# Kernel tuning notes

Hardware: AMD Instinct MI355X
Metric: run time of the kernel (lower is better)

The kernel has to match this reference:

```python
import jax, jax.numpy as jnp
import numpy as np

D_MODEL, H, D_FF = 1024, 16, 4096
D_K = D_MODEL // H
EPS = 1e-6
NEG = -1e9


def _layer_norm(x, alpha, bias):
    # torch LayerNormalization: scalar alpha/bias, unbiased std (ddof=1), eps added to std
    n = x.shape[-1]
    mu = jnp.mean(x, axis=-1, keepdims=True)
    var = jnp.sum((x - mu) ** 2, axis=-1, keepdims=True) / (n - 1)
    std = jnp.sqrt(var)
    return alpha * (x - mu) / (std + EPS) + bias


def _linear(x, w, b):
    # torch nn.Linear: y = x @ W^T + b, W: [out, in]
    return jnp.einsum('bsd,od->bso', x, w) + b


def setup_inputs() -> dict:
    key = jax.random.key(0)
    ks = jax.random.split(key, 12)
    d, dff = D_MODEL, D_FF
    s_d = 1.0 / np.sqrt(d)
    s_ff = 1.0 / np.sqrt(dff)
    inp = {
        'x': jax.random.normal(ks[0], (2, 2048, d), dtype=jnp.float32),
        'mask': jnp.ones((2, 1, 1, 2048), dtype=jnp.int32),
        'wq': jax.random.uniform(ks[1], (d, d), jnp.float32, -s_d, s_d),
        'bq': jnp.zeros((d,), jnp.float32),
        'wk': jax.random.uniform(ks[2], (d, d), jnp.float32, -s_d, s_d),
        'bk': jnp.zeros((d,), jnp.float32),
        'wv': jax.random.uniform(ks[3], (d, d), jnp.float32, -s_d, s_d),
        'bv': jnp.zeros((d,), jnp.float32),
        'wo': jax.random.uniform(ks[4], (d, d), jnp.float32, -s_d, s_d),
        'bo': jnp.zeros((d,), jnp.float32),
        'w1': jax.random.uniform(ks[5], (dff, d), jnp.float32, -s_d, s_d),
        'b1': jnp.zeros((dff,), jnp.float32),
        'w2': jax.random.uniform(ks[6], (d, dff), jnp.float32, -s_ff, s_ff),
        'b2': jnp.zeros((d,), jnp.float32),
        'ln1_a': jnp.ones((1,), jnp.float32),
        'ln1_b': jnp.zeros((1,), jnp.float32),
        'ln2_a': jnp.ones((1,), jnp.float32),
        'ln2_b': jnp.zeros((1,), jnp.float32),
    }
    return inp


def reference(x, mask, wq, bq, wk, bk, wv, bv, wo, bo, w1, b1, w2, b2,
              ln1_a, ln1_b, ln2_a, ln2_b):
    b, s, d = x.shape

    # --- residual 1: pre-norm self-attention (dropout is identity in eval) ---
    xn = _layer_norm(x, ln1_a, ln1_b)
    q = _linear(xn, wq, bq).reshape(b, s, H, D_K).transpose(0, 2, 1, 3)  # [b,h,s,dk]
    k = _linear(xn, wk, bk).reshape(b, s, H, D_K).transpose(0, 2, 1, 3)
    v = _linear(xn, wv, bv).reshape(b, s, H, D_K).transpose(0, 2, 1, 3)
    scores = jnp.einsum('bhqd,bhkd->bhqk', q, k) / jnp.sqrt(jnp.float32(D_K))
    scores = jnp.where(mask == 0, NEG, scores)
    p = jax.nn.softmax(scores, axis=-1)
    attn = jnp.einsum('bhqk,bhkd->bhqd', p, v)
    attn = attn.transpose(0, 2, 1, 3).reshape(b, s, d)
    x = x + _linear(attn, wo, bo)

    # --- residual 2: pre-norm feed-forward ---
    xn = _layer_norm(x, ln2_a, ln2_b)
    h = jax.nn.relu(_linear(xn, w1, b1))
    x = x + _linear(h, w2, b2)
    return x
```

## Files before the change

kernel.cpp:

```cpp
#include <hip/hip_runtime.h>
#include <hip/hip_bf16.h>
#include <stdint.h>

typedef __bf16 bf16x8 __attribute__((ext_vector_type(8)));
typedef __bf16 bf16x4 __attribute__((ext_vector_type(4)));
typedef short  s16x4  __attribute__((ext_vector_type(4)));
typedef float  f32x4  __attribute__((ext_vector_type(4)));
typedef unsigned short u16;

__device__ __forceinline__ u16 f2bf(float f) {
    return __builtin_bit_cast(u16, (__bf16)f);
}

__device__ __forceinline__ f32x4 vmax4(f32x4 a, f32x4 b) {
    f32x4 r;
    r[0] = fmaxf(a[0], b[0]); r[1] = fmaxf(a[1], b[1]);
    r[2] = fmaxf(a[2], b[2]); r[3] = fmaxf(a[3], b[3]);
    return r;
}
__device__ __forceinline__ f32x4 vexp4(f32x4 a) {
    f32x4 r;
    r[0] = __expf(a[0]); r[1] = __expf(a[1]);
    r[2] = __expf(a[2]); r[3] = __expf(a[3]);
    return r;
}

__device__ __forceinline__ f32x4 mfma16(bf16x4 a, bf16x4 b, f32x4 c) {
#if __has_builtin(__builtin_amdgcn_mfma_f32_16x16x16bf16_1k)
    return __builtin_amdgcn_mfma_f32_16x16x16bf16_1k(
        __builtin_bit_cast(s16x4, a), __builtin_bit_cast(s16x4, b), c, 0, 0, 0);
#else
    f32x4 d;
    asm volatile("v_mfma_f32_16x16x16_bf16 %0, %1, %2, %3"
                 : "=v"(d) : "v"(a), "v"(b), "v"(c));
    return d;
#endif
}

__device__ __forceinline__ void stage16(const void* g, void* lds_wave_base) {
#if __has_builtin(__builtin_amdgcn_global_load_lds)
    __builtin_amdgcn_global_load_lds(
        (const __attribute__((address_space(1))) void*)g,
        (__attribute__((address_space(3))) void*)lds_wave_base, 16, 0, 0);
#else
    int lane = threadIdx.x & 63;
    *(uint4*)((char*)lds_wave_base + lane * 16) = *(const uint4*)g;
#endif
}

__device__ __forceinline__ int swz(int r) {
    return (((r) & 7) ^ (((r) >> 3) & 7)) << 4;
}

__global__ void pack1_kernel(const float* __restrict__ wq, const float* __restrict__ wk,
                             const float* __restrict__ wv, const float* __restrict__ bq,
                             const float* __restrict__ bk, const float* __restrict__ bv,
                             const float* __restrict__ wo,
                             u16* __restrict__ wqkv, float* __restrict__ bqkv,
                             u16* __restrict__ wo_b) {
    size_t i0 = (size_t)blockIdx.x * 256 + threadIdx.x;
    size_t stride = (size_t)gridDim.x * 256;
    const size_t DD = 1024u * 1024u;
    for (size_t i = i0; i < 3 * DD; i += stride) {
        float v;
        if (i < DD)          v = wq[i] * 0.125f;
        else if (i < 2 * DD) v = wk[i - DD];
        else                 v = wv[i - 2 * DD];
        wqkv[i] = f2bf(v);
    }
    for (size_t i = i0; i < DD; i += stride) wo_b[i] = f2bf(wo[i]);
    for (size_t i = i0; i < 3072; i += stride)
        bqkv[i] = (i < 1024) ? bq[i] * 0.125f : ((i < 2048) ? bk[i - 1024] : bv[i - 2048]);
}

__global__ void pack2_kernel(const float* __restrict__ w1, const float* __restrict__ w2,
                             u16* __restrict__ w1_b, u16* __restrict__ w2_b) {
    size_t i0 = (size_t)blockIdx.x * 256 + threadIdx.x;
    size_t stride = (size_t)gridDim.x * 256;
    const size_t DD = 1024u * 1024u;
    for (size_t i = i0; i < 4 * DD; i += stride) w1_b[i] = f2bf(w1[i]);
    for (size_t i = i0; i < 4 * DD; i += stride) w2_b[i] = f2bf(w2[i]);
}

__global__ __launch_bounds__(256)
void ln_kernel(const float* __restrict__ x, u16* __restrict__ out,
               const float* __restrict__ alpha, const float* __restrict__ beta) {
    const int row = blockIdx.x;
    const int t = threadIdx.x, lane = t & 63, w = t >> 6;
    float4 v = ((const float4*)(x + (size_t)row * 1024))[t];
    float s  = v.x + v.y + v.z + v.w;
    float ss = v.x * v.x + v.y * v.y + v.z * v.z + v.w * v.w;
#pragma unroll
    for (int d = 1; d < 64; d <<= 1) { s += __shfl_xor(s, d); ss += __shfl_xor(ss, d); }
    __shared__ float red[8];
    if (lane == 0) { red[w] = s; red[4 + w] = ss; }
    __syncthreads();
    s  = red[0] + red[1] + red[2] + red[3];
    ss = red[4] + red[5] + red[6] + red[7];
    const float mu  = s * (1.f / 1024.f);
    const float var = fmaxf((ss - 1024.f * mu * mu) * (1.f / 1023.f), 0.f);
    const float inv = alpha[0] / (sqrtf(var) + 1e-6f);
    const float bb  = beta[0];
    ushort4 o;
    o.x = f2bf((v.x - mu) * inv + bb);
    o.y = f2bf((v.y - mu) * inv + bb);
    o.z = f2bf((v.z - mu) * inv + bb);
    o.w = f2bf((v.w - mu) * inv + bb);
    ((ushort4*)(out + (size_t)row * 1024))[t] = o;
}

template <int EPI>
__global__ __launch_bounds__(256)
void gemm_bt(const u16* __restrict__ A, const u16* __restrict__ B,
             const float* __restrict__ bias, const float* __restrict__ resid,
             void* __restrict__ Cout, int M, int N, int K, int ldc) {
    __shared__ __align__(16) char As[8192];
    __shared__ __align__(16) char Bs[8192];
    const int t = threadIdx.x;
    const int lane = t & 63, wave = t >> 6;
    const int g = lane >> 4, c = lane & 15;
    const int wm = wave >> 1, wn = wave & 1;
    const int bm = blockIdx.x, bn = blockIdx.y;

    const f32x4 z4 = {0.f, 0.f, 0.f, 0.f};
    f32x4 acc[4][4];
#pragma unroll
    for (int m = 0; m < 4; ++m)
#pragma unroll
        for (int n = 0; n < 4; ++n) acc[m][n] = z4;

    const int srow = t >> 2;
    const int ak = (((t & 3) ^ ((t >> 2) & 3)) << 3);
    const u16* ga = A + (size_t)(bm * 128 + srow) * K + ak;
    const u16* gb = B + (size_t)(bn * 128 + srow) * K + ak;
    char* la = As + wave * 1024;
    char* lb = Bs + wave * 1024;
    const size_t rstep = (size_t)64 * K;

    for (int k0 = 0; k0 < K; k0 += 32) {
        __syncthreads();
        stage16(ga + k0,         la);
        stage16(ga + k0 + rstep, la + 4096);
        stage16(gb + k0,         lb);
        stage16(gb + k0 + rstep, lb + 4096);
        __syncthreads();
        bf16x8 a[4], b[4];
#pragma unroll
        for (int m = 0; m < 4; ++m) {
            int r = wm * 64 + m * 16 + c;
            a[m] = *(const bf16x8*)(As + r * 64 + ((g * 16) ^ ((c & 3) << 4)));
        }
#pragma unroll
        for (int n = 0; n < 4; ++n) {
            int r = wn * 64 + n * 16 + c;
            b[n] = *(const bf16x8*)(Bs + r * 64 + ((g * 16) ^ ((c & 3) << 4)));
        }
#pragma unroll
        for (int m = 0; m < 4; ++m)
#pragma unroll
            for (int n = 0; n < 4; ++n)
                acc[m][n] = __builtin_amdgcn_mfma_f32_16x16x32_bf16(a[m], b[n], acc[m][n], 0, 0, 0);
    }

    const int row0 = bm * 128 + wm * 64;
    const int col0 = bn * 128 + wn * 64;
#pragma unroll
    for (int m = 0; m < 4; ++m) {
#pragma unroll
        for (int n = 0; n < 4; ++n) {
            const int cc = col0 + n * 16 + c;
            const float bv = bias[cc];
#pragma unroll
            for (int j = 0; j < 4; ++j) {
                const int rr = row0 + m * 16 + g * 4 + j;
                float v = acc[m][n][j] + bv;
                if (EPI == 1) v = v > 0.f ? v : 0.f;
                if (EPI == 2) {
                    ((float*)Cout)[(size_t)rr * ldc + cc] = resid[(size_t)rr * ldc + cc] + v;
                } else {
                    ((u16*)Cout)[(size_t)rr * ldc + cc] = f2bf(v);
                }
            }
        }
    }
}

__global__ __launch_bounds__(256)
void attn_kernel(const u16* __restrict__ qkv, const int* __restrict__ mask,
                 u16* __restrict__ attn_out) {
    __shared__ __align__(16) char Ksm[32768];
    __shared__ __align__(16) char Vsm[32768];
    const int t = threadIdx.x, lane = t & 63, w = t >> 6;
    const int g = lane >> 4, c = lane & 15;
    const int flat = blockIdx.x;
    const int xcd = flat & 7, u = flat >> 3;
    const int qt = u & 15;
    const int p = xcd * 4 + (u >> 4);
    const int h = p & 15, b = p >> 4;
    const int S = 2048, LD = 3072;
    const int NT = S / 128;

    bf16x8 qf[2][2];
#pragma unroll
    for (int m = 0; m < 2; ++m)
#pragma unroll
        for (int half = 0; half < 2; ++half)
            qf[m][half] = *(const bf16x8*)&qkv[(size_t)(b * S + qt * 128 + w * 32 + m * 16 + c) * LD
                                               + h * 64 + half * 32 + g * 8];

    const f32x4 z4 = {0.f, 0.f, 0.f, 0.f};
    f32x4 accO[2][4];
#pragma unroll
    for (int m = 0; m < 2; ++m)
#pragma unroll
        for (int dt = 0; dt < 4; ++dt) accO[m][dt] = z4;
    float mrun[2] = {-1e30f, -1e30f};
    float lrun[2] = {0.f, 0.f};

    unsigned vr[2][8];
    const int vd0 = (t & 31) * 2;
    const int vkg[2] = {t >> 5, 8 + (t >> 5)};

    auto STAGEK = [&](int kt, char* Kd) {
#pragma unroll
        for (int it = 0; it < 4; ++it) {
            int idx = it * 256 + t;
            int k = idx >> 3, pp = idx & 7;
            int ps = pp ^ ((k & 7) ^ ((k >> 3) & 7));
            stage16(&qkv[(size_t)(b * S + kt * 128 + k) * LD + 1024 + h * 64 + ps * 8],
                    Kd + (it * 256 + w * 64) * 16);
        }
    };
    auto VLOAD = [&](int kt) {
#pragma unroll
        for (int it = 0; it < 2; ++it) {
            const u16* src = &qkv[(size_t)(b * S + kt * 128 + vkg[it] * 8) * LD + 2048 + h * 64 + vd0];
#pragma unroll
            for (int i = 0; i < 8; ++i)
                vr[it][i] = *(const unsigned*)(src + (size_t)i * LD);
        }
    };
    auto VWRITE = [&](char* Vd) {
#pragma unroll
        for (int it = 0; it < 2; ++it) {
            int d0 = vd0, kg = vkg[it];
            uint4 lo, hi;
            lo.x = (vr[it][0] & 0xffffu) | (vr[it][1] << 16);
            lo.y = (vr[it][2] & 0xffffu) | (vr[it][3] << 16);
            lo.z = (vr[it][4] & 0xffffu) | (vr[it][5] << 16);
            lo.w = (vr[it][6] & 0xffffu) | (vr[it][7] << 16);
            hi.x = (vr[it][0] >> 16) | (vr[it][1] & 0xffff0000u);
            hi.y = (vr[it][2] >> 16) | (vr[it][3] & 0xffff0000u);
            hi.z = (vr[it][4] >> 16) | (vr[it][5] & 0xffff0000u);
            hi.w = (vr[it][6] >> 16) | (vr[it][7] & 0xffff0000u);
            *(uint4*)(Vd + d0 * 256 + ((kg * 16) ^ swz(d0)))           = lo;
            *(uint4*)(Vd + (d0 + 1) * 256 + ((kg * 16) ^ swz(d0 + 1))) = hi;
        }
    };

    STAGEK(0, Ksm);
    VLOAD(0);
    asm volatile("s_waitcnt vmcnt(0)" ::: "memory");
    VWRITE(Vsm);
    __syncthreads();

    int cur = 0;
    for (int kt = 0; kt < NT; ++kt) {
        char* Kc = Ksm + cur * 16384;
        char* Vc = Vsm + cur * 16384;
        if (kt + 1 < NT) {
            STAGEK(kt + 1, Ksm + (cur ^ 1) * 16384);
            VLOAD(kt + 1);
        }

        f32x4 s[2][8];
        __builtin_amdgcn_s_setprio(1);
#pragma unroll
        for (int n = 0; n < 8; ++n) {
            int kr = n * 16 + c;
            bf16x8 k0 = *(const bf16x8*)(Kc + kr * 128 + ((g * 16) ^ swz(kr)));
            bf16x8 k1 = *(const bf16x8*)(Kc + kr * 128 + ((64 + g * 16) ^ swz(kr)));
            s[0][n] = __builtin_amdgcn_mfma_f32_16x16x32_bf16(k0, qf[0][0], z4, 0, 0, 0);
            s[0][n] = __builtin_amdgcn_mfma_f32_16x16x32_bf16(k1, qf[0][1], s[0][n], 0, 0, 0);
            s[1][n] = __builtin_amdgcn_mfma_f32_16x16x32_bf16(k0, qf[1][0], z4, 0, 0, 0);
            s[1][n] = __builtin_amdgcn_mfma_f32_16x16x32_bf16(k1, qf[1][1], s[1][n], 0, 0, 0);
        }
        __builtin_amdgcn_s_setprio(0);
#pragma unroll
        for (int n = 0; n < 8; ++n) {
            int4 mv = *(const int4*)&mask[b * S + kt * 128 + n * 16 + g * 4];
            if (mv.x == 0) { s[0][n][0] = -1e9f; s[1][n][0] = -1e9f; }
            if (mv.y == 0) { s[0][n][1] = -1e9f; s[1][n][1] = -1e9f; }
            if (mv.z == 0) { s[0][n][2] = -1e9f; s[1][n][2] = -1e9f; }
            if (mv.w == 0) { s[0][n][3] = -1e9f; s[1][n][3] = -1e9f; }
        }
#pragma unroll
        for (int m = 0; m < 2; ++m) {
            f32x4 pm4 = s[m][0];
#pragma unroll
            for (int n = 1; n < 8; ++n) pm4 = vmax4(pm4, s[m][n]);
            float pm = fmaxf(fmaxf(pm4[0], pm4[1]), fmaxf(pm4[2], pm4[3]));
            pm = fmaxf(pm, __shfl_xor(pm, 16));
            pm = fmaxf(pm, __shfl_xor(pm, 32));
            float mn = fmaxf(mrun[m], pm);
            float sc = __expf(mrun[m] - mn);
            mrun[m] = mn;
            f32x4 mn4 = {mn, mn, mn, mn};
            f32x4 ps4 = z4;
#pragma unroll
            for (int n = 0; n < 8; ++n) { s[m][n] = vexp4(s[m][n] - mn4); ps4 += s[m][n]; }
            float ps = ps4[0] + ps4[1] + ps4[2] + ps4[3];
            ps += __shfl_xor(ps, 16);
            ps += __shfl_xor(ps, 32);
            lrun[m] = lrun[m] * sc + ps;
#pragma unroll
            for (int dt = 0; dt < 4; ++dt) accO[m][dt] *= sc;
        }
        __builtin_amdgcn_s_setprio(1);
#pragma unroll
        for (int n = 0; n < 8; ++n) {
            bf16x4 p0, p1;
#pragma unroll
            for (int j = 0; j < 4; ++j) { p0[j] = (__bf16)s[0][n][j]; p1[j] = (__bf16)s[1][n][j]; }
#pragma unroll
            for (int dt = 0; dt < 4; ++dt) {
                int d = dt * 16 + c;
                bf16x4 vf = *(const bf16x4*)(Vc + d * 256 + ((n * 32 + g * 8) ^ swz(d)));
                accO[0][dt] = mfma16(vf, p0, accO[0][dt]);
                accO[1][dt] = mfma16(vf, p1, accO[1][dt]);
            }
        }
        __builtin_amdgcn_s_setprio(0);

        asm volatile("s_waitcnt vmcnt(0)" ::: "memory");
        if (kt + 1 < NT) VWRITE(Vsm + (cur ^ 1) * 16384);
        __syncthreads();
        cur ^= 1;
    }

    char* Osm = Ksm;
#pragma unroll
    for (int m = 0; m < 2; ++m) {
        float inv = 1.f / lrun[m];
#pragma unroll
        for (int dt = 0; dt < 4; ++dt)
#pragma unroll
            for (int j = 0; j < 4; ++j) {
                int ql = w * 32 + m * 16 + c;
                int d = dt * 16 + g * 4 + j;
                *(u16*)(Osm + ql * 128 + ((d * 2) ^ swz(ql))) = f2bf(accO[m][dt][j] * inv);
            }
    }
    __syncthreads();
#pragma unroll
    for (int it = 0; it < 4; ++it) {
        int idx = it * 256 + t;
        int q = idx >> 3, pp = idx & 7;
        uint4 val = *(const uint4*)(Osm + q * 128 + ((pp * 16) ^ swz(q)));
        *(uint4*)&attn_out[(size_t)(b * S + qt * 128 + q) * 1024 + h * 64 + pp * 8] = val;
    }
}

extern "C" void kernel_launch(void* const* d_in, const int* in_sizes, int n_in,
                              void* d_out, int out_size, void* d_ws, size_t ws_size,
                              hipStream_t stream) {
    const float* x    = (const float*)d_in[0];
    const int*   mask = (const int*)d_in[1];
    const float* wq   = (const float*)d_in[2];
    const float* bq   = (const float*)d_in[3];
    const float* wk   = (const float*)d_in[4];
    const float* bk   = (const float*)d_in[5];
    const float* wv   = (const float*)d_in[6];
    const float* bv   = (const float*)d_in[7];
    const float* wo   = (const float*)d_in[8];
    const float* bo   = (const float*)d_in[9];
    const float* w1   = (const float*)d_in[10];
    const float* b1   = (const float*)d_in[11];
    const float* w2   = (const float*)d_in[12];
    const float* b2   = (const float*)d_in[13];
    const float* ln1a = (const float*)d_in[14];
    const float* ln1b = (const float*)d_in[15];
    const float* ln2a = (const float*)d_in[16];
    const float* ln2b = (const float*)d_in[17];

    const size_t MB = 1048576;
    char* ws = (char*)d_ws;
    const bool big = ws_size >= 88 * MB;

    u16 *xn, *wqkv, *wo_b, *qkvb, *attnb, *w1_b, *w2_b, *hbuf;
    float *bqkv, *x1;
    int nchunk;
    if (big) {
        xn    = (u16*)(ws + 0 * MB);
        wqkv  = (u16*)(ws + 8 * MB);
        wo_b  = (u16*)(ws + 14 * MB);
        qkvb  = (u16*)(ws + 16 * MB);
        attnb = (u16*)(ws + 40 * MB);
        x1    = (float*)(ws + 48 * MB);
        w1_b  = (u16*)(ws + 64 * MB);
        w2_b  = (u16*)(ws + 72 * MB);
        hbuf  = (u16*)(ws + 16 * MB);
        bqkv  = (float*)(ws + 80 * MB);
        nchunk = 1;
    } else {
        xn    = (u16*)(ws + 0 * MB);
        wqkv  = (u16*)(ws + 8 * MB);
        wo_b  = (u16*)(ws + 14 * MB);
        qkvb  = (u16*)(ws + 16 * MB);
        attnb = (u16*)(ws + 40 * MB);
        x1    = (float*)(ws + 16 * MB);
        w1_b  = (u16*)(ws + 32 * MB);
        w2_b  = (u16*)(ws + 8 * MB);
        hbuf  = (u16*)(ws + 40 * MB);
        bqkv  = (float*)(ws + 40 * MB);
        nchunk = 4;
    }

    pack1_kernel<<<1024, 256, 0, stream>>>(wq, wk, wv, bq, bk, bv, wo, wqkv, bqkv, wo_b);
    ln_kernel<<<4096, 256, 0, stream>>>(x, xn, ln1a, ln1b);
    gemm_bt<0><<<dim3(32, 24), 256, 0, stream>>>(xn, wqkv, bqkv, nullptr, qkvb,
                                                 4096, 3072, 1024, 3072);
    attn_kernel<<<512, 256, 0, stream>>>(qkvb, mask, attnb);
    gemm_bt<2><<<dim3(32, 8), 256, 0, stream>>>(attnb, wo_b, bo, x, x1,
                                                4096, 1024, 1024, 1024);
    pack2_kernel<<<1024, 256, 0, stream>>>(w1, w2, w1_b, w2_b);
    ln_kernel<<<4096, 256, 0, stream>>>(x1, xn, ln2a, ln2b);

    const int mrows = 4096 / nchunk;
    for (int cidx = 0; cidx < nchunk; ++cidx) {
        const size_t ro = (size_t)cidx * mrows;
        gemm_bt<1><<<dim3(mrows / 128, 32), 256, 0, stream>>>(
            xn + ro * 1024, w1_b, b1, nullptr, hbuf, mrows, 4096, 1024, 4096);
        gemm_bt<2><<<dim3(mrows / 128, 8), 256, 0, stream>>>(
            hbuf, w2_b, b2, x1 + ro * 1024, (float*)d_out + ro * 1024,
            mrows, 1024, 4096, 1024);
    }
}
```

Measured before the change: 353.2 us.

## Double-buffer GEMM LDS staging, use exp2 softmax with lazy rescaling

The GEMM now double-buffers its LDS tiles, prefetching the next K slice while the current one feeds MFMA, and drops one barrier per iteration. Wave priority is raised around the MFMA block. In attention, the log2(e) factor is folded into the packed Q weights so softmax can use exp2 directly. The running-max rescale is skipped unless the max grows by more than 8 in log2 units. This trades doubled GEMM LDS use and possibly lower occupancy for overlapped loads, and removes exp and multiply work from the attention inner loop.

```diff
diff --git a/kernel.cpp b/kernel.cpp
--- a/kernel.cpp
+++ b/kernel.cpp
@@ -18,10 +18,10 @@
     r[2] = fmaxf(a[2], b[2]); r[3] = fmaxf(a[3], b[3]);
     return r;
 }
-__device__ __forceinline__ f32x4 vexp4(f32x4 a) {
+__device__ __forceinline__ f32x4 vexp2_4(f32x4 a) {
     f32x4 r;
-    r[0] = __expf(a[0]); r[1] = __expf(a[1]);
-    r[2] = __expf(a[2]); r[3] = __expf(a[3]);
+    r[0] = exp2f(a[0]); r[1] = exp2f(a[1]);
+    r[2] = exp2f(a[2]); r[3] = exp2f(a[3]);
     return r;
 }
 
@@ -58,19 +58,20 @@
                              const float* __restrict__ wo,
                              u16* __restrict__ wqkv, float* __restrict__ bqkv,
                              u16* __restrict__ wo_b) {
+    const float QS = 0.125f * 1.44269504088896f;
     size_t i0 = (size_t)blockIdx.x * 256 + threadIdx.x;
     size_t stride = (size_t)gridDim.x * 256;
     const size_t DD = 1024u * 1024u;
     for (size_t i = i0; i < 3 * DD; i += stride) {
         float v;
-        if (i < DD)          v = wq[i] * 0.125f;
+        if (i < DD)          v = wq[i] * QS;
         else if (i < 2 * DD) v = wk[i - DD];
         else                 v = wv[i - 2 * DD];
         wqkv[i] = f2bf(v);
     }
     for (size_t i = i0; i < DD; i += stride) wo_b[i] = f2bf(wo[i]);
     for (size_t i = i0; i < 3072; i += stride)
-        bqkv[i] = (i < 1024) ? bq[i] * 0.125f : ((i < 2048) ? bk[i - 1024] : bv[i - 2048]);
+        bqkv[i] = (i < 1024) ? bq[i] * QS : ((i < 2048) ? bk[i - 1024] : bv[i - 2048]);
 }
 
 __global__ void pack2_kernel(const float* __restrict__ w1, const float* __restrict__ w2,
@@ -114,8 +115,8 @@
 void gemm_bt(const u16* __restrict__ A, const u16* __restrict__ B,
              const float* __restrict__ bias, const float* __restrict__ resid,
              void* __restrict__ Cout, int M, int N, int K, int ldc) {
-    __shared__ __align__(16) char As[8192];
-    __shared__ __align__(16) char Bs[8192];
+    __shared__ __align__(16) char As[16384];
+    __shared__ __align__(16) char Bs[16384];
     const int t = threadIdx.x;
     const int lane = t & 63, wave = t >> 6;
     const int g = lane >> 4, c = lane & 15;
@@ -133,33 +134,47 @@
     const int ak = (((t & 3) ^ ((t >> 2) & 3)) << 3);
     const u16* ga = A + (size_t)(bm * 128 + srow) * K + ak;
     const u16* gb = B + (size_t)(bn * 128 + srow) * K + ak;
-    char* la = As + wave * 1024;
-    char* lb = Bs + wave * 1024;
     const size_t rstep = (size_t)64 * K;
 
-    for (int k0 = 0; k0 < K; k0 += 32) {
-        __syncthreads();
+    auto STAGE = [&](int k0, int buf) {
+        char* la = As + buf * 8192 + wave * 1024;
+        char* lb = Bs + buf * 8192 + wave * 1024;
         stage16(ga + k0,         la);
         stage16(ga + k0 + rstep, la + 4096);
         stage16(gb + k0,         lb);
         stage16(gb + k0 + rstep, lb + 4096);
-        __syncthreads();
+    };
+
+    STAGE(0, 0);
+    asm volatile("s_waitcnt vmcnt(0)" ::: "memory");
+    __syncthreads();
+
+    int cur = 0;
+    for (int k0 = 0; k0 < K; k0 += 32) {
+        if (k0 + 32 < K) STAGE(k0 + 32, cur ^ 1);
+        const char* Ac = As + cur * 8192;
+        const char* Bc = Bs + cur * 8192;
         bf16x8 a[4], b[4];
 #pragma unroll
         for (int m = 0; m < 4; ++m) {
             int r = wm * 64 + m * 16 + c;
-            a[m] = *(const bf16x8*)(As + r * 64 + ((g * 16) ^ ((c & 3) << 4)));
+            a[m] = *(const bf16x8*)(Ac + r * 64 + ((g * 16) ^ ((c & 3) << 4)));
         }
 #pragma unroll
         for (int n = 0; n < 4; ++n) {
             int r = wn * 64 + n * 16 + c;
-            b[n] = *(const bf16x8*)(Bs + r * 64 + ((g * 16) ^ ((c & 3) << 4)));
-        }
+            b[n] = *(const bf16x8*)(Bc + r * 64 + ((g * 16) ^ ((c & 3) << 4)));
+        }
+        __builtin_amdgcn_s_setprio(1);
 #pragma unroll
         for (int m = 0; m < 4; ++m)
 #pragma unroll
             for (int n = 0; n < 4; ++n)
                 acc[m][n] = __builtin_amdgcn_mfma_f32_16x16x32_bf16(a[m], b[n], acc[m][n], 0, 0, 0);
+        __builtin_amdgcn_s_setprio(0);
+        asm volatile("s_waitcnt vmcnt(0)" ::: "memory");
+        __syncthreads();
+        cur ^= 1;
     }
 
     const int row0 = bm * 128 + wm * 64;
@@ -302,19 +317,22 @@
             float pm = fmaxf(fmaxf(pm4[0], pm4[1]), fmaxf(pm4[2], pm4[3]));
             pm = fmaxf(pm, __shfl_xor(pm, 16));
             pm = fmaxf(pm, __shfl_xor(pm, 32));
-            float mn = fmaxf(mrun[m], pm);
-            float sc = __expf(mrun[m] - mn);
-            mrun[m] = mn;
-            f32x4 mn4 = {mn, mn, mn, mn};
+            if (!__all(pm - mrun[m] <= 8.f)) {
+                float mn = fmaxf(mrun[m], pm);
+                float sc = exp2f(mrun[m] - mn);
+                mrun[m] = mn;
+                lrun[m] *= sc;
+#pragma unroll
+                for (int dt = 0; dt < 4; ++dt) accO[m][dt] *= sc;
+            }
+            f32x4 mn4 = {mrun[m], mrun[m], mrun[m], mrun[m]};
             f32x4 ps4 = z4;
 #pragma unroll
-            for (int n = 0; n < 8; ++n) { s[m][n] = vexp4(s[m][n] - mn4); ps4 += s[m][n]; }
+            for (int n = 0; n < 8; ++n) { s[m][n] = vexp2_4(s[m][n] - mn4); ps4 += s[m][n]; }
             float ps = ps4[0] + ps4[1] + ps4[2] + ps4[3];
             ps += __shfl_xor(ps, 16);
             ps += __shfl_xor(ps, 32);
-            lrun[m] = lrun[m] * sc + ps;
-#pragma unroll
-            for (int dt = 0; dt < 4; ++dt) accO[m][dt] *= sc;
+            lrun[m] += ps;
         }
         __builtin_amdgcn_s_setprio(1);
 #pragma unroll
```

Result: faster. 341.8 us (-3.2%).
